# Kernel tuning notes

Hardware: AMD Instinct MI355X
Metric: run time of the kernel (lower is better)

The kernel has to match this reference:

```python
import jax, jax.numpy as jnp
import numpy as np

N, E = 50000, 400000          # nodes, edges
IN, H, OUT = 256, 512, 256    # channels
L, K = 2, 2                   # num_layers, Chebyshev order


def setup_inputs() -> dict:
    key = jax.random.key(0)
    ks = jax.random.split(key, 8)
    x = jax.random.normal(ks[0], (N, IN), jnp.float32)
    edge_index = jax.random.randint(ks[1], (2, E), 0, N)
    in_w = jax.random.normal(ks[2], (IN, H), jnp.float32) / np.float32(np.sqrt(IN))
    in_b = jnp.zeros((H,), jnp.float32)
    # ChebConv has K bias-free Linear layers per conv plus one bias vector
    conv_w = jax.random.normal(ks[3], (L, K, H, H), jnp.float32) / np.float32(np.sqrt(H))
    conv_b = jnp.zeros((L, H), jnp.float32)
    out_w = jax.random.normal(ks[4], (H, OUT), jnp.float32) / np.float32(np.sqrt(H))
    out_b = jnp.zeros((OUT,), jnp.float32)
    return dict(x=x, edge_index=edge_index, in_w=in_w, in_b=in_b,
                conv_w=conv_w, conv_b=conv_b, out_w=out_w, out_b=out_b)


def reference(x, edge_index, in_w, in_b, conv_w, conv_b, out_w, out_b):
    # PyG ChebConv normalization with lambda_max=2 (default):
    #   L_hat = 2/lambda_max * (I - D^{-1/2} A D^{-1/2}) - I = -D^{-1/2} A D^{-1/2}
    # i.e. off-diagonal weights -dinv[row]*w*dinv[col], diagonal 0.
    row, col = edge_index[0], edge_index[1]
    w = jnp.ones((E,), x.dtype)
    deg = jax.ops.segment_sum(w, row, num_segments=N)
    dinv = jnp.where(deg > 0, jax.lax.rsqrt(jnp.maximum(deg, 1e-12)), 0.0).astype(x.dtype)
    norm = -dinv[row] * w * dinv[col]  # [E]

    def prop(h):  # L_hat @ h  (gather from source row, scatter-add to target col)
        return jax.ops.segment_sum(norm[:, None] * h[row], col, num_segments=N)

    # dropout is identity in eval mode; reference is deterministic (eval)
    h = jax.nn.silu(x @ in_w + in_b)
    for l in range(L):
        # Chebyshev recursion, K=2: out = Tx0 @ W0 + (L_hat Tx0) @ W1 + b
        Tx0 = h
        out = Tx0 @ conv_w[l, 0]
        Tx1 = prop(Tx0)
        out = out + Tx1 @ conv_w[l, 1] + conv_b[l]
        h = jax.nn.silu(out)
    return h @ out_w + out_b
```

## Files before the change

### kernel.cpp

```cpp
#include <hip/hip_runtime.h>

#define H512 512

typedef short bf16x8 __attribute__((ext_vector_type(8)));
typedef float f32x4  __attribute__((ext_vector_type(4)));

__device__ __forceinline__ float silu_f(float v) { return v / (1.0f + __expf(-v)); }

__device__ __forceinline__ short f2bf(float f) {
    unsigned u = __float_as_uint(f);
    u = (u + 0x7FFFu + ((u >> 16) & 1u)) >> 16;
    return (short)u;
}
__device__ __forceinline__ float bf2f(short s) {
    return __uint_as_float(((unsigned)(unsigned short)s) << 16);
}

__device__ __forceinline__ int xcd_swz(int b, int nwg) {
    const int NX = 8;
    int q = nwg / NX, rr = nwg % NX;
    int xcd = b % NX, idx = b / NX;
    int base = (xcd < rr) ? xcd * (q + 1) : rr * (q + 1) + (xcd - rr) * q;
    return base + idx;
}


__global__ void hist_kernel(const int* __restrict__ row, const int* __restrict__ col,
                            float* __restrict__ deg, int* __restrict__ cnt, int E) {
    int e = blockIdx.x * blockDim.x + threadIdx.x;
    if (e < E) {
        atomicAdd(&deg[row[e]], 1.0f);
        atomicAdd(&cnt[col[e]], 1);
    }
}

__global__ void dinv_kernel(const float* __restrict__ deg, float* __restrict__ dinv, int n) {
    int i = blockIdx.x * blockDim.x + threadIdx.x;
    if (i < n) {
        float d = deg[i];
        dinv[i] = d > 0.0f ? rsqrtf(fmaxf(d, 1e-12f)) : 0.0f;
    }
}

__global__ __launch_bounds__(256) void bsum_kernel(const int* __restrict__ cnt,
                                                   int* __restrict__ bsum, int n) {
    __shared__ int s[4];
    int i = blockIdx.x * 256 + threadIdx.x;
    int v = (i < n) ? cnt[i] : 0;
    #pragma unroll
    for (int off = 32; off; off >>= 1) v += __shfl_down(v, off, 64);
    if ((threadIdx.x & 63) == 0) s[threadIdx.x >> 6] = v;
    __syncthreads();
    if (threadIdx.x == 0) bsum[blockIdx.x] = s[0] + s[1] + s[2] + s[3];
}

__global__ __launch_bounds__(256) void bscan_kernel(const int* __restrict__ bsum,
                                                    int* __restrict__ boff, int B) {
    __shared__ int s[256];
    int tid = threadIdx.x;
    int v = (tid < B) ? bsum[tid] : 0;
    s[tid] = v;
    __syncthreads();
    #pragma unroll
    for (int off = 1; off < 256; off <<= 1) {
        int t = (tid >= off) ? s[tid - off] : 0;
        __syncthreads();
        s[tid] += t;
        __syncthreads();
    }
    if (tid < B) boff[tid] = s[tid] - v;
}

__global__ __launch_bounds__(256) void cscan_kernel(const int* __restrict__ cnt,
                                                    const int* __restrict__ boff,
                                                    int* __restrict__ ptr,
                                                    int* __restrict__ ptr2, int n, int B) {
    __shared__ int s[256];
    int b = blockIdx.x, tid = threadIdx.x;
    int i = b * 256 + tid;
    int v = (i < n) ? cnt[i] : 0;
    s[tid] = v;
    __syncthreads();
    #pragma unroll
    for (int off = 1; off < 256; off <<= 1) {
        int t = (tid >= off) ? s[tid - off] : 0;
        __syncthreads();
        s[tid] += t;
        __syncthreads();
    }
    int exc = boff[b] + s[tid] - v;
    if (i < n) { ptr[i] = exc; ptr2[i] = exc; }
    if (b == B - 1 && tid == 255) ptr[n] = exc + v;
}

__global__ void scatter_kernel(const int* __restrict__ row, const int* __restrict__ col,
                               const float* __restrict__ dinv, int* __restrict__ ptr2,
                               int* __restrict__ esrc, float* __restrict__ ew, int E) {
    int e = blockIdx.x * blockDim.x + threadIdx.x;
    if (e >= E) return;
    int r = row[e], c = col[e];
    int pos = atomicAdd(&ptr2[c], 1);
    esrc[pos] = r;
    ew[pos]   = -dinv[r] * dinv[c];
}


__device__ __forceinline__ void bfshuf_body(const float* W, short* Bf,
                                            int Ksrc, int Nw, int ktot, int ktoff,
                                            int tid) {
    const int nchunks_src = (Nw / 128) * 2 * (Ksrc / 64) * 8;
    if (tid >= nchunks_src * 64) return;
    int lane = tid & 63;  int rest = tid >> 6;
    int nfrag = rest & 3; rest >>= 2;
    int ks    = rest & 1; rest >>= 1;
    int ktl   = rest % (Ksrc / 64); rest /= (Ksrc / 64);
    int wn    = rest & 1;
    int n128  = rest >> 1;
    int r = lane & 15, g = lane >> 4;
    int colw = n128 * 128 + wn * 64 + nfrag * 16 + r;
    int k0   = ktl * 64 + ks * 32 + g * 8;
    size_t dst = ((size_t)(((n128 * 2 + wn) * ktot + ktoff + ktl) * 8 + ks * 4 + nfrag) * 64 + lane) * 8;
    bf16x8 o;
    #pragma unroll
    for (int j = 0; j < 8; ++j) o[j] = f2bf(W[(size_t)(k0 + j) * Nw + colw]);
    *(bf16x8*)(Bf + dst) = o;
}

__global__ void bfshuf_kernel(const float* __restrict__ W, short* __restrict__ Bf,
                              int Ksrc, int Nw, int ktot, int ktoff) {
    bfshuf_body(W, Bf, Ksrc, Nw, ktot, ktoff, blockIdx.x * blockDim.x + threadIdx.x);
}

__global__ void bfshuf4_kernel(const float* __restrict__ Wall, short* __restrict__ Bf) {
    int li = blockIdx.y;
    bfshuf_body(Wall + (size_t)li * 512 * 512,
                Bf + (size_t)(li >> 1) * 512 * 1024,
                512, 512, 16, (li & 1) * 8,
                blockIdx.x * blockDim.x + threadIdx.x);
}

__global__ void xconv_kernel(const float* __restrict__ x, short* __restrict__ xb,
                             int Nreal, int Mpad) {
    int tid = blockIdx.x * blockDim.x + threadIdx.x;
    if (tid >= Mpad * 32) return;
    int r = tid >> 5, c8 = (tid & 31) * 8;
    bf16x8 o = {0, 0, 0, 0, 0, 0, 0, 0};
    if (r < Nreal) {
        const float4 f0 = *(const float4*)(x + (size_t)r * 256 + c8);
        const float4 f1 = *(const float4*)(x + (size_t)r * 256 + c8 + 4);
        o[0] = f2bf(f0.x); o[1] = f2bf(f0.y); o[2] = f2bf(f0.z); o[3] = f2bf(f0.w);
        o[4] = f2bf(f1.x); o[5] = f2bf(f1.y); o[6] = f2bf(f1.z); o[7] = f2bf(f1.w);
    }
    *(bf16x8*)(xb + (size_t)r * 256 + c8) = o;
}


__global__ __launch_bounds__(256) void gather_kernel(
    const int* __restrict__ ptr, const int* __restrict__ esrc,
    const float* __restrict__ ew, const short* __restrict__ T,
    short* __restrict__ U, int Nreal, int Mpad)
{
    int t = threadIdx.x;
    int node = blockIdx.x * 4 + (t >> 6);
    if (node >= Mpad) return;
    int q = (t & 63) * 8;
    if (node >= Nreal) {
        bf16x8 z = {0, 0, 0, 0, 0, 0, 0, 0};
        *(bf16x8*)(U + (size_t)node * H512 + q) = z;
        return;
    }
    float a0[8] = {}, a1[8] = {}, a2[8] = {}, a3[8] = {};
    float a4[8] = {}, a5[8] = {}, a6[8] = {}, a7[8] = {};
    int i = ptr[node];
    const int i1 = ptr[node + 1];
    for (; i + 8 <= i1; i += 8) {
        int s0 = esrc[i],     s1 = esrc[i + 1], s2 = esrc[i + 2], s3 = esrc[i + 3];
        int s4 = esrc[i + 4], s5 = esrc[i + 5], s6 = esrc[i + 6], s7 = esrc[i + 7];
        float w0 = ew[i],     w1 = ew[i + 1], w2 = ew[i + 2], w3 = ew[i + 3];
        float w4 = ew[i + 4], w5 = ew[i + 5], w6 = ew[i + 6], w7 = ew[i + 7];
        bf16x8 t0 = *(const bf16x8*)(T + (size_t)s0 * H512 + q);
        bf16x8 t1 = *(const bf16x8*)(T + (size_t)s1 * H512 + q);
        bf16x8 t2 = *(const bf16x8*)(T + (size_t)s2 * H512 + q);
        bf16x8 t3 = *(const bf16x8*)(T + (size_t)s3 * H512 + q);
        bf16x8 t4 = *(const bf16x8*)(T + (size_t)s4 * H512 + q);
        bf16x8 t5 = *(const bf16x8*)(T + (size_t)s5 * H512 + q);
        bf16x8 t6 = *(const bf16x8*)(T + (size_t)s6 * H512 + q);
        bf16x8 t7 = *(const bf16x8*)(T + (size_t)s7 * H512 + q);
        #pragma unroll
        for (int j = 0; j < 8; ++j) {
            a0[j] += w0 * bf2f(t0[j]);
            a1[j] += w1 * bf2f(t1[j]);
            a2[j] += w2 * bf2f(t2[j]);
            a3[j] += w3 * bf2f(t3[j]);
            a4[j] += w4 * bf2f(t4[j]);
            a5[j] += w5 * bf2f(t5[j]);
            a6[j] += w6 * bf2f(t6[j]);
            a7[j] += w7 * bf2f(t7[j]);
        }
    }
    for (; i + 4 <= i1; i += 4) {
        int s0 = esrc[i], s1 = esrc[i + 1], s2 = esrc[i + 2], s3 = esrc[i + 3];
        float w0 = ew[i], w1 = ew[i + 1], w2 = ew[i + 2], w3 = ew[i + 3];
        bf16x8 t0 = *(const bf16x8*)(T + (size_t)s0 * H512 + q);
        bf16x8 t1 = *(const bf16x8*)(T + (size_t)s1 * H512 + q);
        bf16x8 t2 = *(const bf16x8*)(T + (size_t)s2 * H512 + q);
        bf16x8 t3 = *(const bf16x8*)(T + (size_t)s3 * H512 + q);
        #pragma unroll
        for (int j = 0; j < 8; ++j) {
            a0[j] += w0 * bf2f(t0[j]);
            a1[j] += w1 * bf2f(t1[j]);
            a2[j] += w2 * bf2f(t2[j]);
            a3[j] += w3 * bf2f(t3[j]);
        }
    }
    for (; i < i1; ++i) {
        int s   = esrc[i];
        float w = ew[i];
        bf16x8 tv = *(const bf16x8*)(T + (size_t)s * H512 + q);
        #pragma unroll
        for (int j = 0; j < 8; ++j) a0[j] += w * bf2f(tv[j]);
    }
    bf16x8 o;
    #pragma unroll
    for (int j = 0; j < 8; ++j)
        o[j] = f2bf(((a0[j] + a1[j]) + (a2[j] + a3[j])) + ((a4[j] + a5[j]) + (a6[j] + a7[j])));
    *(bf16x8*)(U + (size_t)node * H512 + q) = o;
}


template<int SILU, int F32OUT>
__global__ __launch_bounds__(256, 4) void mfma_gemm(
    const short* __restrict__ A0, const short* __restrict__ A1, int ksplit, int lda,
    const short* __restrict__ Bf,
    void* __restrict__ Cout, int ldc,
    const float* __restrict__ bias, int Mreal, int K, int gx)
{
    __shared__ alignas(16) short As[2][128 * 64];

    const int t    = threadIdx.x;
    const int lane = t & 63;
    const int wid  = t >> 6;

    const int wg = xcd_swz(blockIdx.x, gridDim.x);
    const int m0 = (wg / gx) * 128;
    const int n0 = (wg % gx) * 128;

    const int wm = wid >> 1;
    const int wn = wid & 1;

    const int srow  = lane >> 3;
    const int scol  = (lane & 7) * 16;
    const int corig = scol ^ (srow << 4);
    const int cel   = corig >> 1;

    const int r = lane & 15;
    const int g = lane >> 4;

    const int nt = K >> 6;
    const short* Bw = Bf + (size_t)((n0 >> 7) * 2 + wn) * nt * 4096;

    f32x4 acc[4][4];
    #pragma unroll
    for (int m = 0; m < 4; ++m)
        #pragma unroll
        for (int n = 0; n < 4; ++n)
            acc[m][n] = (f32x4){0.f, 0.f, 0.f, 0.f};

    auto stageA = [&](int buf, int kt) {
        const int k0 = kt * 64;
        const short* Abase = (k0 < ksplit) ? (A0 + k0) : (A1 + (k0 - ksplit));
        #pragma unroll
        for (int i = 0; i < 4; ++i) {
            const int r0 = (wid * 4 + i) * 8;
            const short* ga = Abase + (size_t)(m0 + r0 + srow) * lda + cel;
            __builtin_amdgcn_global_load_lds(
                (const __attribute__((address_space(1))) void*)ga,
                (__attribute__((address_space(3))) void*)(As[buf] + r0 * 64), 16, 0, 0);
        }
    };
    auto loadB = [&](bf16x8* bb, int kt) {
        #pragma unroll
        for (int ks = 0; ks < 2; ++ks)
            #pragma unroll
            for (int n = 0; n < 4; ++n)
                bb[ks * 4 + n] = *(const bf16x8*)(Bw + (size_t)(kt * 8 + ks * 4 + n) * 512 + lane * 8);
    };
    auto mmstep = [&](int cur, const bf16x8* bb) {
        const short* Ab = As[cur];
        #pragma unroll
        for (int ks = 0; ks < 2; ++ks) {
            bf16x8 af[4];
            #pragma unroll
            for (int m = 0; m < 4; ++m) {
                const int rowA = wm * 64 + m * 16 + r;
                const int cb   = (ks * 64 + g * 16) ^ ((rowA & 7) << 4);
                af[m] = *(const bf16x8*)((const char*)Ab + rowA * 128 + cb);
            }
            #pragma unroll
            for (int m = 0; m < 4; ++m)
                #pragma unroll
                for (int n = 0; n < 4; ++n)
                    acc[m][n] = __builtin_amdgcn_mfma_f32_16x16x32_bf16(
                        af[m], bb[ks * 4 + n], acc[m][n], 0, 0, 0);
        }
    };

    bf16x8 b[8];
    stageA(0, 0);
    stageA(1, 1);
    loadB(b, 0);
    __builtin_amdgcn_sched_barrier(0);

    for (int tt = 0; tt < nt; ++tt) {
        if (tt + 1 < nt) asm volatile("s_waitcnt vmcnt(12)" ::: "memory");
        else             asm volatile("s_waitcnt vmcnt(8)"  ::: "memory");
        __builtin_amdgcn_s_barrier();
        __builtin_amdgcn_sched_barrier(0);
        mmstep(tt & 1, b);
        __builtin_amdgcn_sched_barrier(0);
        __builtin_amdgcn_s_barrier();
        if (tt + 1 < nt) loadB(b, tt + 1);
        if (tt + 2 < nt) stageA(tt & 1, tt + 2);
        __builtin_amdgcn_sched_barrier(0);
    }

    float bb2[4];
    #pragma unroll
    for (int n = 0; n < 4; ++n) bb2[n] = bias[n0 + wn * 64 + n * 16 + r];

    if (F32OUT) {
        #pragma unroll
        for (int m = 0; m < 4; ++m)
            #pragma unroll
            for (int j = 0; j < 4; ++j) {
                const int rr = m0 + wm * 64 + m * 16 + g * 4 + j;
                #pragma unroll
                for (int n = 0; n < 4; ++n) {
                    float v = acc[m][n][j] + bb2[n];
                    if (SILU) v = silu_f(v);
                    if (rr < Mreal)
                        ((float*)Cout)[(size_t)rr * ldc + n0 + wn * 64 + n * 16 + r] = v;
                }
            }
    } else {
        __syncthreads();
        short* fs = (short*)As;
        #pragma unroll
        for (int m = 0; m < 4; ++m)
            #pragma unroll
            for (int j = 0; j < 4; ++j) {
                const int row = wm * 64 + m * 16 + g * 4 + j;
                const int rot = (row & 15) << 3;
                #pragma unroll
                for (int n = 0; n < 4; ++n) {
                    float v = acc[m][n][j] + bb2[n];
                    if (SILU) v = silu_f(v);
                    const int col = wn * 64 + n * 16 + r;
                    fs[row * 128 + ((col + rot) & 127)] = f2bf(v);
                }
            }
        __syncthreads();
        const int rr   = t >> 1;
        const int hf   = t & 1;
        const int rot2 = (rr & 15) << 3;
        const size_t gr = (size_t)(m0 + rr);
        #pragma unroll
        for (int c8 = 0; c8 < 8; ++c8) {
            const int cbase = hf * 64 + c8 * 8;
            const int cl    = (cbase + rot2) & 127;
            bf16x8 v8 = *(const bf16x8*)&fs[rr * 128 + cl];
            *(bf16x8*)((short*)Cout + gr * ldc + n0 + cbase) = v8;
        }
    }
}


extern "C" void kernel_launch(void* const* d_in, const int* in_sizes, int n_in,
                              void* d_out, int out_size, void* d_ws, size_t ws_size,
                              hipStream_t stream)
{
    const float* x      = (const float*)d_in[0];
    const int*   ei     = (const int*)  d_in[1];
    const float* in_w   = (const float*)d_in[2];
    const float* in_b   = (const float*)d_in[3];
    const float* conv_w = (const float*)d_in[4];
    const float* conv_b = (const float*)d_in[5];
    const float* out_w  = (const float*)d_in[6];
    const float* out_b  = (const float*)d_in[7];

    const int N = in_sizes[0] / 256;
    const int E = in_sizes[1] / 2;
    const int MPAD = ((N + 127) / 128) * 128;
    const int* row = ei;
    const int* col = ei + E;

    char* p = (char*)d_ws;
    short* h0 = (short*)p; p += (size_t)MPAD * H512 * 2;
    short* h1 = (short*)p; p += (size_t)MPAD * H512 * 2;
    short* G  = (short*)p; p += (size_t)MPAD * H512 * 2;
    short* xb = G;
    short* bfi = (short*)p; p += (size_t)512 * 256 * 2;
    short* bfc = (short*)p; p += (size_t)2 * 512 * 1024 * 2;
    short* bfo = (short*)p; p += (size_t)256 * 512 * 2;
    float* deg  = (float*)p; p += (size_t)N * 4;
    float* dinv = (float*)p; p += (size_t)N * 4;
    float* ew   = (float*)p; p += (size_t)E * 4;
    int*   cnt  = (int*)p;   p += (size_t)N * 4;
    int*   ptr  = (int*)p;   p += (size_t)(N + 4) * 4;
    int*   ptr2 = (int*)p;   p += (size_t)N * 4;
    int*   esrc = (int*)p;   p += (size_t)E * 4;
    int*   bsum = (int*)p;   p += (size_t)256 * 4;
    int*   boff = (int*)p;   p += (size_t)256 * 4;

    const int NB = (N + 255) / 256;

    hipMemsetAsync(deg, 0, (size_t)N * sizeof(float), stream);
    hipMemsetAsync(cnt, 0, (size_t)N * sizeof(int), stream);
    hist_kernel<<<(E + 255) / 256, 256, 0, stream>>>(row, col, deg, cnt, E);
    dinv_kernel<<<(N + 255) / 256, 256, 0, stream>>>(deg, dinv, N);
    bsum_kernel <<<NB, 256, 0, stream>>>(cnt, bsum, N);
    bscan_kernel<<<1, 256, 0, stream>>>(bsum, boff, NB);
    cscan_kernel<<<NB, 256, 0, stream>>>(cnt, boff, ptr, ptr2, N, NB);
    scatter_kernel<<<(E + 255) / 256, 256, 0, stream>>>(row, col, dinv, ptr2, esrc, ew, E);

    bfshuf_kernel<<<(512 * 256 / 8 + 255) / 256, 256, 0, stream>>>(in_w, bfi, 256, 512, 4, 0);
    bfshuf4_kernel<<<dim3((512 * 512 / 8 + 255) / 256, 4), 256, 0, stream>>>(conv_w, bfc);
    bfshuf_kernel<<<(512 * 256 / 8 + 255) / 256, 256, 0, stream>>>(out_w, bfo, 512, 256, 8, 0);
    xconv_kernel<<<(MPAD * 32 + 255) / 256, 256, 0, stream>>>(x, xb, N, MPAD);

    const int mt = MPAD / 128;

    mfma_gemm<1, 0><<<dim3(4 * mt), 256, 0, stream>>>(
        xb, xb, 256, 256, bfi, h0, H512, in_b, N, 256, 4);

    short* hc = h0;
    short* hn = h1;
    for (int l = 0; l < 2; ++l) {
        gather_kernel<<<(MPAD + 3) / 4, 256, 0, stream>>>(ptr, esrc, ew, hc, G, N, MPAD);
        mfma_gemm<1, 0><<<dim3(4 * mt), 256, 0, stream>>>(
            hc, G, 512, H512, bfc + (size_t)l * 512 * 1024,
            hn, H512, conv_b + (size_t)l * H512, N, 1024, 4);
        short* tmp = hc; hc = hn; hn = tmp;
    }

    mfma_gemm<0, 1><<<dim3(2 * mt), 256, 0, stream>>>(
        hc, hc, 512, H512, bfo, d_out, 256, out_b, N, 512, 2);
}
```

Baseline: 436.3 us.

## Triple-buffer A tiles in LDS and double-buffer B registers in MFMA GEMM

The GEMM main loop moves from a two-slot LDS buffer for A and one B register set to a rotating three-slot LDS ring and two B register sets, unrolled by two. Loads for step s+2 are issued right after step s's compute, so the second barrier per iteration goes away and more memory traffic overlaps with compute. The cost is 48KB of LDS per block and higher register pressure from the extra B fragments, so launch bounds drop to three blocks per CU, which lowers occupancy. The wait counts assume an even number of k-tiles.

New measurement: 586.6 us. 1.34x slower.

```diff
diff --git a/kernel.cpp b/kernel.cpp
--- a/kernel.cpp
+++ b/kernel.cpp
@@ -229,13 +229,13 @@
 
 
 template<int SILU, int F32OUT>
-__global__ __launch_bounds__(256, 4) void mfma_gemm(
+__global__ __launch_bounds__(256, 3) void mfma_gemm(
     const short* __restrict__ A0, const short* __restrict__ A1, int ksplit, int lda,
     const short* __restrict__ Bf,
     void* __restrict__ Cout, int ldc,
     const float* __restrict__ bias, int Mreal, int K, int gx)
 {
-    __shared__ alignas(16) short As[2][128 * 64];
+    __shared__ alignas(16) short lds3[3 * 128 * 64];
 
     const int t    = threadIdx.x;
     const int lane = t & 63;
@@ -266,7 +266,7 @@
         for (int n = 0; n < 4; ++n)
             acc[m][n] = (f32x4){0.f, 0.f, 0.f, 0.f};
 
-    auto stageA = [&](int buf, int kt) {
+    auto stageA = [&](int coff, int kt) {
         const int k0 = kt * 64;
         const short* Abase = (k0 < ksplit) ? (A0 + k0) : (A1 + (k0 - ksplit));
         #pragma unroll
@@ -275,7 +275,7 @@
             const short* ga = Abase + (size_t)(m0 + r0 + srow) * lda + cel;
             __builtin_amdgcn_global_load_lds(
                 (const __attribute__((address_space(1))) void*)ga,
-                (__attribute__((address_space(3))) void*)(As[buf] + r0 * 64), 16, 0, 0);
+                (__attribute__((address_space(3))) void*)(lds3 + coff + r0 * 64), 16, 0, 0);
         }
     };
     auto loadB = [&](bf16x8* bb, int kt) {
@@ -285,8 +285,8 @@
             for (int n = 0; n < 4; ++n)
                 bb[ks * 4 + n] = *(const bf16x8*)(Bw + (size_t)(kt * 8 + ks * 4 + n) * 512 + lane * 8);
     };
-    auto mmstep = [&](int cur, const bf16x8* bb) {
-        const short* Ab = As[cur];
+    auto mmstep = [&](int coff, const bf16x8* bb) {
+        const short* Ab = lds3 + coff;
         #pragma unroll
         for (int ks = 0; ks < 2; ++ks) {
             bf16x8 af[4];
@@ -305,22 +305,32 @@
         }
     };
 
-    bf16x8 b[8];
-    stageA(0, 0);
-    stageA(1, 1);
-    loadB(b, 0);
+    bf16x8 bE[8], bO[8];
+    int c0 = 0, c1 = 8192, c2 = 16384;
+    stageA(c0, 0);
+    loadB(bE, 0);
+    stageA(c1, 1);
+    loadB(bO, 1);
     __builtin_amdgcn_sched_barrier(0);
 
-    for (int tt = 0; tt < nt; ++tt) {
-        if (tt + 1 < nt) asm volatile("s_waitcnt vmcnt(12)" ::: "memory");
-        else             asm volatile("s_waitcnt vmcnt(8)"  ::: "memory");
+    for (int s = 0; s < nt; s += 2) {
+        if (s + 1 < nt) asm volatile("s_waitcnt vmcnt(12)" ::: "memory");
+        else            asm volatile("s_waitcnt vmcnt(0)"  ::: "memory");
         __builtin_amdgcn_s_barrier();
         __builtin_amdgcn_sched_barrier(0);
-        mmstep(tt & 1, b);
-        __builtin_amdgcn_sched_barrier(0);
+        mmstep(c0, bE);
+        __builtin_amdgcn_sched_barrier(0);
+        if (s + 2 < nt) { stageA(c2, s + 2); loadB(bE, s + 2); }
+        { int tmp = c0; c0 = c1; c1 = c2; c2 = tmp; }
+        __builtin_amdgcn_sched_barrier(0);
+        if (s + 2 < nt) asm volatile("s_waitcnt vmcnt(12)" ::: "memory");
+        else            asm volatile("s_waitcnt vmcnt(0)"  ::: "memory");
         __builtin_amdgcn_s_barrier();
-        if (tt + 1 < nt) loadB(b, tt + 1);
-        if (tt + 2 < nt) stageA(tt & 1, tt + 2);
+        __builtin_amdgcn_sched_barrier(0);
+        mmstep(c0, bO);
+        __builtin_amdgcn_sched_barrier(0);
+        if (s + 3 < nt) { stageA(c2, s + 3); loadB(bO, s + 3); }
+        { int tmp = c0; c0 = c1; c1 = c2; c2 = tmp; }
         __builtin_amdgcn_sched_barrier(0);
     }
 
@@ -344,7 +354,7 @@
             }
     } else {
         __syncthreads();
-        short* fs = (short*)As;
+        short* fs = (short*)lds3;
         #pragma unroll
         for (int m = 0; m < 4; ++m)
             #pragma unroll
```
